# Optimization experiments

Hardware: AMD Instinct MI355X
Metric: run time of the kernel (lower is better)

Reference implementation:

```python
import jax, jax.numpy as jnp
import numpy as np


def setup_inputs() -> dict:
    key = jax.random.key(0)
    qkv = jax.random.normal(key, (8, 1536, 2048), dtype=jnp.float32)
    return {"qkv": qkv, "n_heads": 8}


def reference(qkv, n_heads):
    # qkv: [N, H*3*C, T] -> output [N, H*C, T]
    bs, width, length = qkv.shape
    assert width % (3 * n_heads) == 0
    ch = width // (3 * n_heads)
    qkv_r = qkv.reshape(bs * n_heads, 3 * ch, length)
    q, k, v = qkv_r[:, :ch], qkv_r[:, ch:2 * ch], qkv_r[:, 2 * ch:]
    scale = 1.0 / np.sqrt(np.sqrt(ch))  # applied to both q and k
    # [B, T, S] scores
    weight = jnp.einsum('bct,bcs->bts', q * scale, k * scale)
    weight = jax.nn.softmax(weight.astype(jnp.float32), axis=-1).astype(weight.dtype)
    a = jnp.einsum('bts,bcs->bct', weight, v)
    return a.reshape(bs, n_heads * ch, length)
```

## Files before the change

kernel.cpp:

```cpp
#include <hip/hip_runtime.h>


typedef __bf16 bf16;
typedef __bf16 bf16x4 __attribute__((ext_vector_type(4)));
typedef __bf16 bf16x8 __attribute__((ext_vector_type(8)));
typedef float  f32x4  __attribute__((ext_vector_type(4)));
typedef float  f32x16 __attribute__((ext_vector_type(16)));
typedef unsigned int u32;

#define NLEN 2048
#define DCH  64
#define HSTR (NLEN * DCH * 2)
#define WS_K (16u * 1024u * 1024u)
#define WS_V (32u * 1024u * 1024u)
#define WS_NEED (48u * 1024u * 1024u)
#define PSCALE 0.42466119f

__device__ __forceinline__ int swzK(int row, int cb) {
    return row * 128 + ((((cb >> 4) ^ row) & 7) << 4) + (cb & 15);
}
__device__ __forceinline__ int swzO(int row, int cb) {
    int g = cb >> 4;
    g = (g & ~7) | ((g ^ row) & 7);
    return row * 512 + (g << 4) + (cb & 15);
}

__device__ __forceinline__ void gload16(const char* g, char* l) {
    __builtin_amdgcn_global_load_lds((const __attribute__((address_space(1))) void*)g,
                                     (__attribute__((address_space(3))) void*)l, 16, 0, 0);
}

__global__ __launch_bounds__(256)
void prep(const float* __restrict__ qkv, char* __restrict__ ws)
{
    const int tid  = threadIdx.x;
    const int pb   = blockIdx.x;
    const int head = blockIdx.y;
    const int type = blockIdx.z;

    const float* src = qkv + (size_t)head * (3 * DCH) * NLEN + (size_t)type * DCH * NLEN;
    char* dst = ws + (type == 0 ? 0u : (type == 1 ? WS_K : WS_V))
                   + (size_t)head * HSTR + (size_t)pb * 8192;

    if (type < 2) {
        __shared__ float T[64][65];
        #pragma unroll
        for (int p = 0; p < 4; ++p) {
            int idx = tid + p * 256;
            int c = idx >> 4, q4 = idx & 15;
            float4 f = *(const float4*)(src + (size_t)c * NLEN + pb * 64 + q4 * 4);
            T[q4 * 4 + 0][c] = f.x * PSCALE;
            T[q4 * 4 + 1][c] = f.y * PSCALE;
            T[q4 * 4 + 2][c] = f.z * PSCALE;
            T[q4 * 4 + 3][c] = f.w * PSCALE;
        }
        __syncthreads();
        #pragma unroll
        for (int p = 0; p < 2; ++p) {
            int gidx = tid + p * 256;
            int s = gidx >> 3, G = gidx & 7;
            int c0 = (G ^ (s & 7)) * 8;
            bf16 tmp[8];
            #pragma unroll
            for (int j = 0; j < 8; ++j) tmp[j] = (bf16)T[s][c0 + j];
            *(bf16x8*)(dst + s * 128 + G * 16) = *(bf16x8*)tmp;
        }
    } else {
        const int c = tid >> 2, so = (tid & 3) * 16;
        const float* sp = src + (size_t)c * NLEN + pb * 64 + so;
        float f[16];
        #pragma unroll
        for (int j = 0; j < 4; ++j) *(f32x4*)(f + 4 * j) = *(const f32x4*)(sp + 4 * j);
        #pragma unroll
        for (int gl = 0; gl < 2; ++gl) {
            bf16 tmp[8];
            #pragma unroll
            for (int j = 0; j < 8; ++j) tmp[j] = (bf16)f[gl * 8 + j];
            const int Gp = ((so >> 3) + gl) ^ (c & 7);
            *(bf16x8*)(dst + c * 128 + Gp * 16) = *(bf16x8*)tmp;
        }
    }
}

__global__ __launch_bounds__(256, 4)
void attn_main(const char* __restrict__ ws, float* __restrict__ out)
{
    const int tid  = threadIdx.x;
    const int lane = tid & 63;
    const int w    = tid >> 6;
    const int hi   = lane >> 5;
    const int ll5  = lane & 31;

    const int bid  = blockIdx.x;
    const int head = (bid & 7) * 8 + ((bid >> 3) & 7);
    const int tblk = bid >> 6;
    const int t0   = tblk * 128;

    const char* Qb = ws + (size_t)head * HSTR + (size_t)t0 * 128;
    const char* Kb = ws + WS_K + (size_t)head * HSTR;
    const char* Vb = ws + WS_V + (size_t)head * HSTR;

    __shared__ __align__(16) char lds[32768];

    #pragma unroll
    for (int i = 0; i < 4; ++i)
        gload16(Qb + tid * 16 + i * 4096, lds + tid * 16 + i * 4096);
    asm volatile("s_waitcnt vmcnt(0)");
    __syncthreads();

    bf16x8 qf[4];
    #pragma unroll
    for (int kc = 0; kc < 4; ++kc)
        qf[kc] = *(const bf16x8*)(lds + swzK(w * 32 + ll5, kc * 32 + hi * 16));
    __syncthreads();

    gload16(Kb + tid * 16,        lds + tid * 16);
    gload16(Kb + 4096 + tid * 16, lds + 4096 + tid * 16);
    gload16(Vb + tid * 16,        lds + 8192 + tid * 16);
    gload16(Vb + 4096 + tid * 16, lds + 12288 + tid * 16);
    asm volatile("s_waitcnt vmcnt(0)");
    __syncthreads();

    f32x16 o0 = {}, o1 = {};
    float l_r = 0.f;
    int cur = 0;

    for (int sb = 0; sb < 32; ++sb) {
        if (sb < 31) {
            char* bn = lds + (cur ^ 1) * 16384;
            const char* kn = Kb + (size_t)(sb + 1) * 8192;
            const char* vn = Vb + (size_t)(sb + 1) * 8192;
            gload16(kn + tid * 16,        bn + tid * 16);
            gload16(kn + 4096 + tid * 16, bn + 4096 + tid * 16);
            gload16(vn + tid * 16,        bn + 8192 + tid * 16);
            gload16(vn + 4096 + tid * 16, bn + 12288 + tid * 16);
        }
        char* Kc = lds + cur * 16384;
        char* Vc = Kc + 8192;

        f32x16 sf0 = {}, sf1 = {};
        __builtin_amdgcn_s_setprio(1);
        #pragma unroll
        for (int kc = 0; kc < 4; ++kc) {
            bf16x8 a0 = *(const bf16x8*)(Kc + swzK(ll5,      kc * 32 + hi * 16));
            bf16x8 a1 = *(const bf16x8*)(Kc + swzK(32 + ll5, kc * 32 + hi * 16));
            sf0 = __builtin_amdgcn_mfma_f32_32x32x16_bf16(a0, qf[kc], sf0, 0, 0, 0);
            sf1 = __builtin_amdgcn_mfma_f32_32x32x16_bf16(a1, qf[kc], sf1, 0, 0, 0);
        }
        __builtin_amdgcn_s_setprio(0);

        float ps0 = 0.f, ps1 = 0.f, ps2 = 0.f, ps3 = 0.f;
        #pragma unroll
        for (int r = 0; r < 16; r += 4) {
            sf0[r + 0] = __builtin_amdgcn_exp2f(sf0[r + 0]); ps0 += sf0[r + 0];
            sf0[r + 1] = __builtin_amdgcn_exp2f(sf0[r + 1]); ps1 += sf0[r + 1];
            sf0[r + 2] = __builtin_amdgcn_exp2f(sf0[r + 2]); ps2 += sf0[r + 2];
            sf0[r + 3] = __builtin_amdgcn_exp2f(sf0[r + 3]); ps3 += sf0[r + 3];
        }
        #pragma unroll
        for (int r = 0; r < 16; r += 4) {
            sf1[r + 0] = __builtin_amdgcn_exp2f(sf1[r + 0]); ps0 += sf1[r + 0];
            sf1[r + 1] = __builtin_amdgcn_exp2f(sf1[r + 1]); ps1 += sf1[r + 1];
            sf1[r + 2] = __builtin_amdgcn_exp2f(sf1[r + 2]); ps2 += sf1[r + 2];
            sf1[r + 3] = __builtin_amdgcn_exp2f(sf1[r + 3]); ps3 += sf1[r + 3];
        }
        l_r += (ps0 + ps1) + (ps2 + ps3);

        bf16x8 pa[4];
        #pragma unroll
        for (int ks = 0; ks < 4; ++ks) {
            const f32x16& pp = (ks < 2) ? sf0 : sf1;
            const int rb = (ks & 1) * 8;
            u32 X, X2, Y, Y2;
            asm("v_cvt_pk_bf16_f32 %0, %1, %2" : "=v"(X)  : "v"(pp[rb + 0]), "v"(pp[rb + 1]));
            asm("v_cvt_pk_bf16_f32 %0, %1, %2" : "=v"(X2) : "v"(pp[rb + 2]), "v"(pp[rb + 3]));
            asm("v_cvt_pk_bf16_f32 %0, %1, %2" : "=v"(Y)  : "v"(pp[rb + 4]), "v"(pp[rb + 5]));
            asm("v_cvt_pk_bf16_f32 %0, %1, %2" : "=v"(Y2) : "v"(pp[rb + 6]), "v"(pp[rb + 7]));
            asm("v_permlane32_swap_b32 %0, %1" : "+v"(X),  "+v"(Y));
            asm("v_permlane32_swap_b32 %0, %1" : "+v"(X2), "+v"(Y2));
            u32 wds[4] = {X, X2, Y, Y2};
            pa[ks] = *(bf16x8*)wds;
        }

        __builtin_amdgcn_s_setprio(1);
        #pragma unroll
        for (int ks = 0; ks < 4; ++ks) {
            bf16x8 b0 = *(const bf16x8*)(Vc + swzK(ll5,      ks * 32 + hi * 16));
            bf16x8 b1 = *(const bf16x8*)(Vc + swzK(32 + ll5, ks * 32 + hi * 16));
            o0 = __builtin_amdgcn_mfma_f32_32x32x16_bf16(pa[ks], b0, o0, 0, 0, 0);
            o1 = __builtin_amdgcn_mfma_f32_32x32x16_bf16(pa[ks], b1, o1, 0, 0, 0);
        }
        __builtin_amdgcn_s_setprio(0);

        asm volatile("s_waitcnt vmcnt(0)");
        __syncthreads();
        cur ^= 1;
    }

    float lf = l_r + __shfl_xor(l_r, 32);
    float linv = 1.0f / lf;
    float li[16];
    #pragma unroll
    for (int r = 0; r < 16; ++r)
        li[r] = __shfl(linv, (r & 3) + 8 * (r >> 2) + 4 * hi);
    #pragma unroll
    for (int r = 0; r < 16; ++r) { o0[r] *= li[r]; o1[r] *= li[r]; }

    __syncthreads();
    float* Of = (float*)lds;
    #pragma unroll
    for (int j = 0; j < 4; ++j) {
        const int tb = w * 32 + 8 * j + 4 * hi;
        f32x4 v0, v1;
        #pragma unroll
        for (int r = 0; r < 4; ++r) { v0[r] = o0[4 * j + r]; v1[r] = o1[4 * j + r]; }
        *(f32x4*)((char*)Of + swzO(ll5,      tb * 4)) = v0;
        *(f32x4*)((char*)Of + swzO(32 + ll5, tb * 4)) = v1;
    }
    __syncthreads();

    float* op = out + (size_t)head * DCH * NLEN + t0;
    #pragma unroll
    for (int ch = 0; ch < 8; ++ch) {
        const int idx = tid + ch * 256;
        const int c = idx >> 5, tq = idx & 31;
        f32x4 v = *(const f32x4*)((char*)Of + swzO(c, tq * 16));
        *(float4*)(op + (size_t)c * NLEN + tq * 4) = *(float4*)&v;
    }
}

#define CEXP_FB 0.18033688011112042f
#define QSCALE_FB 0.35355339059327373f
__global__ __launch_bounds__(512, 2)
void attn_fwd(const float* __restrict__ qkv, float* __restrict__ out)
{
    const int tid  = threadIdx.x;
    const int lane = tid & 63;
    const int w    = tid >> 6;
    const int lg   = lane >> 4;
    const int ll   = lane & 15;
    const int tblk = blockIdx.x;
    const int head = blockIdx.y;
    const int t0   = tblk * 128;

    const float* qp = qkv + (size_t)head * (3 * DCH) * NLEN;
    const float* kp = qp + (size_t)DCH * NLEN;
    const float* vp = kp + (size_t)DCH * NLEN;

    __shared__ __align__(16) char lds[48 * 1024];
    char* Qs = lds;
    char* Ks = lds + 16 * 1024;
    char* Vs = lds + 24 * 1024;
    char* Ps = lds + 32 * 1024 + w * 2048;

    {
        const int G = tid >> 6;
        #pragma unroll
        for (int it = 0; it < 2; ++it) {
            const int t = (tid & 63) + it * 64;
            const float* src = qp + (size_t)(G * 8) * NLEN + t0 + t;
            bf16 tmp[8];
            #pragma unroll
            for (int j = 0; j < 8; ++j) tmp[j] = (bf16)(src[(size_t)j * NLEN] * QSCALE_FB);
            *(bf16x8*)(Qs + swzK(t, G * 16)) = *(bf16x8*)tmp;
        }
    }
    __syncthreads();
    bf16x8 qf[2];
    #pragma unroll
    for (int kk = 0; kk < 2; ++kk)
        qf[kk] = *(const bf16x8*)(Qs + swzK(w * 16 + ll, kk * 64 + lg * 16));

    f32x4 o[4] = {};
    float m_r = -3.0e38f, l_r = 0.f;

    for (int sb = 0; sb < NLEN / 64; ++sb) {
        const int s0 = sb * 64;
        __syncthreads();
        {
            const int s = tid & 63, G = tid >> 6;
            const float* src = kp + (size_t)(G * 8) * NLEN + s0 + s;
            bf16 tmp[8];
            #pragma unroll
            for (int j = 0; j < 8; ++j) tmp[j] = (bf16)(src[(size_t)j * NLEN] * QSCALE_FB);
            *(bf16x8*)(Ks + swzK(s, G * 16)) = *(bf16x8*)tmp;
        }
        {
            const int c = tid >> 3, s8 = tid & 7;
            const float* src = vp + (size_t)c * NLEN + s0 + s8 * 8;
            const float4 f0 = *(const float4*)src;
            const float4 f1 = *(const float4*)(src + 4);
            bf16 tmp[8] = {(bf16)f0.x, (bf16)f0.y, (bf16)f0.z, (bf16)f0.w,
                           (bf16)f1.x, (bf16)f1.y, (bf16)f1.z, (bf16)f1.w};
            *(bf16x8*)(Vs + swzK(c, s8 * 16)) = *(bf16x8*)tmp;
        }
        __syncthreads();

        f32x4 sf[4] = {};
        #pragma unroll
        for (int kk = 0; kk < 2; ++kk)
            #pragma unroll
            for (int fs = 0; fs < 4; ++fs) {
                bf16x8 a = *(const bf16x8*)(Ks + swzK(fs * 16 + ll, kk * 64 + lg * 16));
                sf[fs] = __builtin_amdgcn_mfma_f32_16x16x32_bf16(a, qf[kk], sf[fs], 0, 0, 0);
            }

        float mx;
        {
            f32x4 m4 = sf[0];
            #pragma unroll
            for (int fs = 1; fs < 4; ++fs) {
                m4[0] = fmaxf(m4[0], sf[fs][0]); m4[1] = fmaxf(m4[1], sf[fs][1]);
                m4[2] = fmaxf(m4[2], sf[fs][2]); m4[3] = fmaxf(m4[3], sf[fs][3]);
            }
            mx = fmaxf(fmaxf(m4[0], m4[1]), fmaxf(m4[2], m4[3]));
        }
        mx = fmaxf(mx, __shfl_xor(mx, 16));
        mx = fmaxf(mx, __shfl_xor(mx, 32));
        const float mnew = fmaxf(m_r, mx);
        const float corr = exp2f((m_r - mnew) * 1.4426950408889634f);
        m_r = mnew;
        const float cm = mnew * 1.4426950408889634f;

        float psum = 0.f;
        #pragma unroll
        for (int fs = 0; fs < 4; ++fs) {
            bf16x4 pw;
            #pragma unroll
            for (int r = 0; r < 4; ++r) {
                float p = exp2f(fmaf(sf[fs][r], 1.4426950408889634f, -cm));
                psum += p;
                pw[r] = (bf16)p;
            }
            *(bf16x4*)(Ps + swzK(ll, 32 * fs + 8 * lg)) = pw;
        }
        psum += __shfl_xor(psum, 16);
        psum += __shfl_xor(psum, 32);
        l_r = l_r * corr + psum;

        float corr4[4];
        #pragma unroll
        for (int r = 0; r < 4; ++r) corr4[r] = __shfl(corr, 4 * lg + r);
        #pragma unroll
        for (int cf = 0; cf < 4; ++cf)
            #pragma unroll
            for (int r = 0; r < 4; ++r) o[cf][r] *= corr4[r];

        #pragma unroll
        for (int kk = 0; kk < 2; ++kk) {
            bf16x8 pa = *(const bf16x8*)(Ps + swzK(ll, kk * 64 + lg * 16));
            #pragma unroll
            for (int cf = 0; cf < 4; ++cf) {
                bf16x8 b = *(const bf16x8*)(Vs + swzK(cf * 16 + ll, kk * 64 + lg * 16));
                o[cf] = __builtin_amdgcn_mfma_f32_16x16x32_bf16(pa, b, o[cf], 0, 0, 0);
            }
        }
    }

    __syncthreads();
    const float linv = 1.0f / l_r;
    float linv4[4];
    #pragma unroll
    for (int r = 0; r < 4; ++r) linv4[r] = __shfl(linv, 4 * lg + r);
    float* Of = (float*)lds;
    #pragma unroll
    for (int cf = 0; cf < 4; ++cf) {
        f32x4 ov;
        #pragma unroll
        for (int r = 0; r < 4; ++r) ov[r] = o[cf][r] * linv4[r];
        *(f32x4*)((char*)Of + swzO(cf * 16 + ll, (w * 16 + 4 * lg) * 4)) = ov;
    }
    __syncthreads();
    float* op = out + (size_t)head * DCH * NLEN + t0;
    #pragma unroll
    for (int it = 0; it < 4; ++it) {
        const int idx = tid + it * 512;
        const int c = idx >> 5, tq = idx & 31;
        f32x4 v = *(const f32x4*)((char*)Of + swzO(c, tq * 16));
        *(float4*)(op + (size_t)c * NLEN + tq * 4) = *(float4*)&v;
    }
}

extern "C" void kernel_launch(void* const* d_in, const int* in_sizes, int n_in,
                              void* d_out, int out_size, void* d_ws, size_t ws_size,
                              hipStream_t stream)
{
    const float* qkv = (const float*)d_in[0];
    float* out = (float*)d_out;
    if (ws_size >= (size_t)WS_NEED) {
        char* ws = (char*)d_ws;
        prep<<<dim3(32, 64, 3), 256, 0, stream>>>(qkv, ws);
        attn_main<<<dim3(1024), 256, 0, stream>>>(ws, out);
    } else {
        attn_fwd<<<dim3(16, 64), 512, 0, stream>>>(qkv, out);
    }
}
```

Before: 106.8 us.

## Double query rows per wave to reuse K/V tiles across two Q blocks

```diff
diff --git a/kernel.cpp b/kernel.cpp
--- a/kernel.cpp
+++ b/kernel.cpp
@@ -82,7 +82,7 @@
     }
 }
 
-__global__ __launch_bounds__(256, 4)
+__global__ __launch_bounds__(256, 2)
 void attn_main(const char* __restrict__ ws, float* __restrict__ out)
 {
     const int tid  = threadIdx.x;
@@ -94,7 +94,7 @@
     const int bid  = blockIdx.x;
     const int head = (bid & 7) * 8 + ((bid >> 3) & 7);
     const int tblk = bid >> 6;
-    const int t0   = tblk * 128;
+    const int t0   = tblk * 256;
 
     const char* Qb = ws + (size_t)head * HSTR + (size_t)t0 * 128;
     const char* Kb = ws + WS_K + (size_t)head * HSTR;
@@ -103,15 +103,17 @@
     __shared__ __align__(16) char lds[32768];
 
     #pragma unroll
-    for (int i = 0; i < 4; ++i)
+    for (int i = 0; i < 8; ++i)
         gload16(Qb + tid * 16 + i * 4096, lds + tid * 16 + i * 4096);
     asm volatile("s_waitcnt vmcnt(0)");
     __syncthreads();
 
-    bf16x8 qf[4];
-    #pragma unroll
-    for (int kc = 0; kc < 4; ++kc)
-        qf[kc] = *(const bf16x8*)(lds + swzK(w * 32 + ll5, kc * 32 + hi * 16));
+    bf16x8 qf0[4], qf1[4];
+    #pragma unroll
+    for (int kc = 0; kc < 4; ++kc) {
+        qf0[kc] = *(const bf16x8*)(lds + swzK(w * 64 + ll5,      kc * 32 + hi * 16));
+        qf1[kc] = *(const bf16x8*)(lds + swzK(w * 64 + 32 + ll5, kc * 32 + hi * 16));
+    }
     __syncthreads();
 
     gload16(Kb + tid * 16,        lds + tid * 16);
@@ -121,8 +123,8 @@
     asm volatile("s_waitcnt vmcnt(0)");
     __syncthreads();
 
-    f32x16 o0 = {}, o1 = {};
-    float l_r = 0.f;
+    f32x16 o00 = {}, o01 = {}, o10 = {}, o11 = {};
+    float l0 = 0.f, l1 = 0.f;
     int cur = 0;
 
     for (int sb = 0; sb < 32; ++sb) {
@@ -138,48 +140,76 @@
         char* Kc = lds + cur * 16384;
         char* Vc = Kc + 8192;
 
-        f32x16 sf0 = {}, sf1 = {};
+        f32x16 s00 = {}, s10 = {}, s01 = {}, s11 = {};
         __builtin_amdgcn_s_setprio(1);
         #pragma unroll
         for (int kc = 0; kc < 4; ++kc) {
             bf16x8 a0 = *(const bf16x8*)(Kc + swzK(ll5,      kc * 32 + hi * 16));
             bf16x8 a1 = *(const bf16x8*)(Kc + swzK(32 + ll5, kc * 32 + hi * 16));
-            sf0 = __builtin_amdgcn_mfma_f32_32x32x16_bf16(a0, qf[kc], sf0, 0, 0, 0);
-            sf1 = __builtin_amdgcn_mfma_f32_32x32x16_bf16(a1, qf[kc], sf1, 0, 0, 0);
+            s00 = __builtin_amdgcn_mfma_f32_32x32x16_bf16(a0, qf0[kc], s00, 0, 0, 0);
+            s10 = __builtin_amdgcn_mfma_f32_32x32x16_bf16(a1, qf0[kc], s10, 0, 0, 0);
+            s01 = __builtin_amdgcn_mfma_f32_32x32x16_bf16(a0, qf1[kc], s01, 0, 0, 0);
+            s11 = __builtin_amdgcn_mfma_f32_32x32x16_bf16(a1, qf1[kc], s11, 0, 0, 0);
         }
         __builtin_amdgcn_s_setprio(0);
 
-        float ps0 = 0.f, ps1 = 0.f, ps2 = 0.f, ps3 = 0.f;
-        #pragma unroll
-        for (int r = 0; r < 16; r += 4) {
-            sf0[r + 0] = __builtin_amdgcn_exp2f(sf0[r + 0]); ps0 += sf0[r + 0];
-            sf0[r + 1] = __builtin_amdgcn_exp2f(sf0[r + 1]); ps1 += sf0[r + 1];
-            sf0[r + 2] = __builtin_amdgcn_exp2f(sf0[r + 2]); ps2 += sf0[r + 2];
-            sf0[r + 3] = __builtin_amdgcn_exp2f(sf0[r + 3]); ps3 += sf0[r + 3];
-        }
-        #pragma unroll
-        for (int r = 0; r < 16; r += 4) {
-            sf1[r + 0] = __builtin_amdgcn_exp2f(sf1[r + 0]); ps0 += sf1[r + 0];
-            sf1[r + 1] = __builtin_amdgcn_exp2f(sf1[r + 1]); ps1 += sf1[r + 1];
-            sf1[r + 2] = __builtin_amdgcn_exp2f(sf1[r + 2]); ps2 += sf1[r + 2];
-            sf1[r + 3] = __builtin_amdgcn_exp2f(sf1[r + 3]); ps3 += sf1[r + 3];
-        }
-        l_r += (ps0 + ps1) + (ps2 + ps3);
-
-        bf16x8 pa[4];
-        #pragma unroll
-        for (int ks = 0; ks < 4; ++ks) {
-            const f32x16& pp = (ks < 2) ? sf0 : sf1;
-            const int rb = (ks & 1) * 8;
-            u32 X, X2, Y, Y2;
-            asm("v_cvt_pk_bf16_f32 %0, %1, %2" : "=v"(X)  : "v"(pp[rb + 0]), "v"(pp[rb + 1]));
-            asm("v_cvt_pk_bf16_f32 %0, %1, %2" : "=v"(X2) : "v"(pp[rb + 2]), "v"(pp[rb + 3]));
-            asm("v_cvt_pk_bf16_f32 %0, %1, %2" : "=v"(Y)  : "v"(pp[rb + 4]), "v"(pp[rb + 5]));
-            asm("v_cvt_pk_bf16_f32 %0, %1, %2" : "=v"(Y2) : "v"(pp[rb + 6]), "v"(pp[rb + 7]));
-            asm("v_permlane32_swap_b32 %0, %1" : "+v"(X),  "+v"(Y));
-            asm("v_permlane32_swap_b32 %0, %1" : "+v"(X2), "+v"(Y2));
-            u32 wds[4] = {X, X2, Y, Y2};
-            pa[ks] = *(bf16x8*)wds;
+        {
+            float a = 0.f, b = 0.f, c = 0.f, d = 0.f;
+            #pragma unroll
+            for (int r = 0; r < 16; r += 4) {
+                s00[r+0] = __builtin_amdgcn_exp2f(s00[r+0]); a += s00[r+0];
+                s00[r+1] = __builtin_amdgcn_exp2f(s00[r+1]); b += s00[r+1];
+                s00[r+2] = __builtin_amdgcn_exp2f(s00[r+2]); c += s00[r+2];
+                s00[r+3] = __builtin_amdgcn_exp2f(s00[r+3]); d += s00[r+3];
+            }
+            #pragma unroll
+            for (int r = 0; r < 16; r += 4) {
+                s10[r+0] = __builtin_amdgcn_exp2f(s10[r+0]); a += s10[r+0];
+                s10[r+1] = __builtin_amdgcn_exp2f(s10[r+1]); b += s10[r+1];
+                s10[r+2] = __builtin_amdgcn_exp2f(s10[r+2]); c += s10[r+2];
+                s10[r+3] = __builtin_amdgcn_exp2f(s10[r+3]); d += s10[r+3];
+            }
+            l0 += (a + b) + (c + d);
+        }
+        {
+            float a = 0.f, b = 0.f, c = 0.f, d = 0.f;
+            #pragma unroll
+            for (int r = 0; r < 16; r += 4) {
+                s01[r+0] = __builtin_amdgcn_exp2f(s01[r+0]); a += s01[r+0];
+                s01[r+1] = __builtin_amdgcn_exp2f(s01[r+1]); b += s01[r+1];
+                s01[r+2] = __builtin_amdgcn_exp2f(s01[r+2]); c += s01[r+2];
+                s01[r+3] = __builtin_amdgcn_exp2f(s01[r+3]); d += s01[r+3];
+            }
+            #pragma unroll
+            for (int r = 0; r < 16; r += 4) {
+                s11[r+0] = __builtin_amdgcn_exp2f(s11[r+0]); a += s11[r+0];
+                s11[r+1] = __builtin_amdgcn_exp2f(s11[r+1]); b += s11[r+1];
+                s11[r+2] = __builtin_amdgcn_exp2f(s11[r+2]); c += s11[r+2];
+                s11[r+3] = __builtin_amdgcn_exp2f(s11[r+3]); d += s11[r+3];
+            }
+            l1 += (a + b) + (c + d);
+        }
+
+        bf16x8 pa0[4], pa1[4];
+        #pragma unroll
+        for (int th = 0; th < 2; ++th) {
+            const f32x16& sl = th ? s01 : s00;
+            const f32x16& sh = th ? s11 : s10;
+            bf16x8* pa = th ? pa1 : pa0;
+            #pragma unroll
+            for (int ks = 0; ks < 4; ++ks) {
+                const f32x16& pp = (ks < 2) ? sl : sh;
+                const int rb = (ks & 1) * 8;
+                u32 X, X2, Y, Y2;
+                asm("v_cvt_pk_bf16_f32 %0, %1, %2" : "=v"(X)  : "v"(pp[rb + 0]), "v"(pp[rb + 1]));
+                asm("v_cvt_pk_bf16_f32 %0, %1, %2" : "=v"(X2) : "v"(pp[rb + 2]), "v"(pp[rb + 3]));
+                asm("v_cvt_pk_bf16_f32 %0, %1, %2" : "=v"(Y)  : "v"(pp[rb + 4]), "v"(pp[rb + 5]));
+                asm("v_cvt_pk_bf16_f32 %0, %1, %2" : "=v"(Y2) : "v"(pp[rb + 6]), "v"(pp[rb + 7]));
+                asm("v_permlane32_swap_b32 %0, %1" : "+v"(X),  "+v"(Y));
+                asm("v_permlane32_swap_b32 %0, %1" : "+v"(X2), "+v"(Y2));
+                u32 wds[4] = {X, X2, Y, Y2};
+                pa[ks] = *(bf16x8*)wds;
+            }
         }
 
         __builtin_amdgcn_s_setprio(1);
@@ -187,8 +217,10 @@
         for (int ks = 0; ks < 4; ++ks) {
             bf16x8 b0 = *(const bf16x8*)(Vc + swzK(ll5,      ks * 32 + hi * 16));
             bf16x8 b1 = *(const bf16x8*)(Vc + swzK(32 + ll5, ks * 32 + hi * 16));
-            o0 = __builtin_amdgcn_mfma_f32_32x32x16_bf16(pa[ks], b0, o0, 0, 0, 0);
-            o1 = __builtin_amdgcn_mfma_f32_32x32x16_bf16(pa[ks], b1, o1, 0, 0, 0);
+            o00 = __builtin_amdgcn_mfma_f32_32x32x16_bf16(pa0[ks], b0, o00, 0, 0, 0);
+            o01 = __builtin_amdgcn_mfma_f32_32x32x16_bf16(pa0[ks], b1, o01, 0, 0, 0);
+            o10 = __builtin_amdgcn_mfma_f32_32x32x16_bf16(pa1[ks], b0, o10, 0, 0, 0);
+            o11 = __builtin_amdgcn_mfma_f32_32x32x16_bf16(pa1[ks], b1, o11, 0, 0, 0);
         }
         __builtin_amdgcn_s_setprio(0);
 
@@ -197,35 +229,54 @@
         cur ^= 1;
     }
 
-    float lf = l_r + __shfl_xor(l_r, 32);
-    float linv = 1.0f / lf;
-    float li[16];
-    #pragma unroll
-    for (int r = 0; r < 16; ++r)
-        li[r] = __shfl(linv, (r & 3) + 8 * (r >> 2) + 4 * hi);
-    #pragma unroll
-    for (int r = 0; r < 16; ++r) { o0[r] *= li[r]; o1[r] *= li[r]; }
-
-    __syncthreads();
+    const float lf0 = l0 + __shfl_xor(l0, 32);
+    const float lf1 = l1 + __shfl_xor(l1, 32);
+    const float li0 = 1.0f / lf0;
+    const float li1 = 1.0f / lf1;
+    float a0[16], a1[16];
+    #pragma unroll
+    for (int r = 0; r < 16; ++r) {
+        const int src = (r & 3) + 8 * (r >> 2) + 4 * hi;
+        a0[r] = __shfl(li0, src);
+        a1[r] = __shfl(li1, src);
+    }
+    #pragma unroll
+    for (int r = 0; r < 16; ++r) {
+        o00[r] *= a0[r]; o01[r] *= a0[r];
+        o10[r] *= a1[r]; o11[r] *= a1[r];
+    }
+
+    float* op = out + (size_t)head * DCH * NLEN + t0;
     float* Of = (float*)lds;
-    #pragma unroll
-    for (int j = 0; j < 4; ++j) {
-        const int tb = w * 32 + 8 * j + 4 * hi;
-        f32x4 v0, v1;
-        #pragma unroll
-        for (int r = 0; r < 4; ++r) { v0[r] = o0[4 * j + r]; v1[r] = o1[4 * j + r]; }
-        *(f32x4*)((char*)Of + swzO(ll5,      tb * 4)) = v0;
-        *(f32x4*)((char*)Of + swzO(32 + ll5, tb * 4)) = v1;
-    }
-    __syncthreads();
-
-    float* op = out + (size_t)head * DCH * NLEN + t0;
-    #pragma unroll
-    for (int ch = 0; ch < 8; ++ch) {
-        const int idx = tid + ch * 256;
-        const int c = idx >> 5, tq = idx & 31;
-        f32x4 v = *(const f32x4*)((char*)Of + swzO(c, tq * 16));
-        *(float4*)(op + (size_t)c * NLEN + tq * 4) = *(float4*)&v;
+
+    #pragma unroll
+    for (int p = 0; p < 2; ++p) {
+        __syncthreads();
+        if ((w >> 1) == p) {
+            const int wl = w & 1;
+            #pragma unroll
+            for (int th = 0; th < 2; ++th) {
+                const f32x16& v0 = th ? o10 : o00;
+                const f32x16& v1 = th ? o11 : o01;
+                #pragma unroll
+                for (int j = 0; j < 4; ++j) {
+                    const int tb = wl * 64 + th * 32 + 8 * j + 4 * hi;
+                    f32x4 u0, u1;
+                    #pragma unroll
+                    for (int r = 0; r < 4; ++r) { u0[r] = v0[4 * j + r]; u1[r] = v1[4 * j + r]; }
+                    *(f32x4*)((char*)Of + swzO(ll5,      tb * 4)) = u0;
+                    *(f32x4*)((char*)Of + swzO(32 + ll5, tb * 4)) = u1;
+                }
+            }
+        }
+        __syncthreads();
+        #pragma unroll
+        for (int ch = 0; ch < 8; ++ch) {
+            const int idx = tid + ch * 256;
+            const int c = idx >> 5, tq = idx & 31;
+            f32x4 v = *(const f32x4*)((char*)Of + swzO(c, tq * 16));
+            *(float4*)(op + (size_t)c * NLEN + p * 128 + tq * 4) = *(float4*)&v;
+        }
     }
 }
 
@@ -390,7 +441,7 @@
     if (ws_size >= (size_t)WS_NEED) {
         char* ws = (char*)d_ws;
         prep<<<dim3(32, 64, 3), 256, 0, stream>>>(qkv, ws);
-        attn_main<<<dim3(1024), 256, 0, stream>>>(ws, out);
+        attn_main<<<dim3(512), 256, 0, stream>>>(ws, out);
     } else {
         attn_fwd<<<dim3(16, 64), 512, 0, stream>>>(qkv, out);
     }
```

Result: faster. 101.1 us (-5.3%).
